# Optimization experiments

Hardware: AMD Instinct MI355X
Metric: run time of the kernel (lower is better)

Reference implementation:

```python
import jax, jax.numpy as jnp
import numpy as np

WS = 7
NUM_HEADS = 4


def setup_inputs() -> dict:
    key = jax.random.key(0)
    ks = jax.random.split(key, 5)
    C = 128
    return {
        "x": jax.random.normal(ks[0], (8, 222, 222, C), dtype=jnp.float32),
        "qkv_w": jax.random.normal(ks[1], (C, 3 * C), dtype=jnp.float32) * 0.02,
        "qkv_b": jax.random.normal(ks[2], (3 * C,), dtype=jnp.float32) * 0.02,
        "proj_w": jax.random.normal(ks[3], (C, C), dtype=jnp.float32) * 0.02,
        "proj_b": jax.random.normal(ks[4], (C,), dtype=jnp.float32) * 0.02,
    }


def reference(x, qkv_w, qkv_b, proj_w, proj_b):
    B, H, W, C = x.shape
    ws, nh = WS, NUM_HEADS
    hd = C // nh
    scale = hd ** (-0.5)
    pad_h = (ws - H % ws) % ws
    pad_w = (ws - W % ws) % ws
    xp = jnp.pad(x, ((0, 0), (0, pad_h), (0, pad_w), (0, 0)))
    Hp, Wp = H + pad_h, W + pad_w
    # window partition: [B,Hp,Wp,C] -> [nW, ws*ws, C]
    xw = xp.reshape(B, Hp // ws, ws, Wp // ws, ws, C)
    xw = xw.transpose(0, 1, 3, 2, 4, 5).reshape(-1, ws * ws, C)
    # qkv projection
    qkv = xw @ qkv_w + qkv_b  # [nW, 49, 3C]
    qkv = qkv.reshape(-1, ws * ws, 3, nh, hd).transpose(2, 0, 3, 1, 4)
    q, k, v = qkv[0], qkv[1], qkv[2]  # each [nW, nh, 49, hd]
    attn = jax.nn.softmax(jnp.einsum('whqd,whkd->whqk', q, k) * scale, axis=-1)
    out = jnp.einsum('whqk,whkd->whqd', attn, v)  # [nW, nh, 49, hd]
    out = out.transpose(0, 2, 1, 3).reshape(-1, ws * ws, C)
    out = out @ proj_w + proj_b
    # window reverse: [nW, ws*ws, C] -> [B, Hp, Wp, C]
    out = out.reshape(B, Hp // ws, Wp // ws, ws, ws, C)
    out = out.transpose(0, 1, 3, 2, 4, 5).reshape(B, Hp, Wp, C)
    return out[:, :H, :W, :]
```

## Files before the change

### kernel.cpp

```cpp
#include <hip/hip_runtime.h>
#include <stdint.h>

typedef __attribute__((ext_vector_type(8))) short bf16x8;
typedef __attribute__((ext_vector_type(4))) float f32x4;

#define IMG 222

__device__ __forceinline__ unsigned short f2bf(float f){
  unsigned int u = __float_as_uint(f);
  return (unsigned short)((u + 0x7fffu + ((u >> 16) & 1u)) >> 16);
}

__device__ __forceinline__ int sw128(int r, int c){ return r*128 + (c ^ ((r & 7) << 3)); }
__device__ __forceinline__ int sw64 (int r, int c){ return r*64  + (c ^ ((r & 7) << 3)); }

__global__ void prep_weights(const float* __restrict__ qkv_w,
                             const float* __restrict__ proj_w,
                             unsigned short* __restrict__ qwt,
                             unsigned short* __restrict__ pwt){
  int i = blockIdx.x * blockDim.x + threadIdx.x;
  if (i < 384*128){ int n = i >> 7, k = i & 127; qwt[i] = f2bf(qkv_w[k*384 + n]); }
  if (i < 128*128){ int n = i >> 7, k = i & 127; pwt[i] = f2bf(proj_w[k*128 + n]); }
}

__global__ __launch_bounds__(256, 3)
void win_attn(const float* __restrict__ x,
              const float* __restrict__ qkv_b,
              const float* __restrict__ proj_b,
              const unsigned short* __restrict__ qwt,
              const unsigned short* __restrict__ pwt,
              float* __restrict__ out)
{
  extern __shared__ unsigned short lds[];
  unsigned short* r0 = lds;
  unsigned short* r1 = lds + 8192;
  unsigned short* r2 = lds + 16384;

  const int tid = threadIdx.x;
  const int wid = tid >> 6;
  const int l   = tid & 63;
  const int l15 = l & 15;
  const int lhi = l >> 4;

  const int w  = (blockIdx.x & 7) * 1024 + (blockIdx.x >> 3);
  const int b  = w >> 10;
  const int wi = (w >> 5) & 31;
  const int wj = w & 31;

  {
    const int t  = tid >> 2;
    const int cb = (tid & 3) * 32;
    const int r  = t / 7, c = t - r*7;
    const int gh = wi*7 + r, gw = wj*7 + c;
    const bool valid = (t < 49) && (gh < IMG) && (gw < IMG);
    const float* src = x + (((size_t)((size_t)b*IMG + gh))*IMG + gw)*128 + cb;
    #pragma unroll
    for (int i = 0; i < 8; ++i){
      float4 v = valid ? *(const float4*)(src + i*4) : make_float4(0.f,0.f,0.f,0.f);
      *(ushort4*)(r0 + sw128(t, cb + i*4)) =
        make_ushort4(f2bf(v.x), f2bf(v.y), f2bf(v.z), f2bf(v.w));
    }
  }
  __syncthreads();

  bf16x8 a[4][4];
  #pragma unroll
  for (int mi = 0; mi < 4; ++mi)
    #pragma unroll
    for (int ks = 0; ks < 4; ++ks)
      a[mi][ks] = *(const bf16x8*)(r0 + sw128(mi*16 + l15, ks*32 + lhi*8));
  __syncthreads();

  const float scale = 0.17677669529663687f;

  #pragma unroll
  for (int nj = 0; nj < 6; ++nj){
    const int ni = wid + nj*4;
    bf16x8 bfr[4];
    #pragma unroll
    for (int ks = 0; ks < 4; ++ks)
      bfr[ks] = *(const bf16x8*)(qwt + (ni*16 + l15)*128 + ks*32 + lhi*8);
    if (nj < 4){
      const float4 bias4 = *(const float4*)(qkv_b + ni*16 + lhi*4);
      #pragma unroll
      for (int mi = 0; mi < 4; ++mi){
        f32x4 acc = {0.f,0.f,0.f,0.f};
        #pragma unroll
        for (int ks = 0; ks < 4; ++ks)
          acc = __builtin_amdgcn_mfma_f32_16x16x32_bf16(bfr[ks], a[mi][ks], acc, 0, 0, 0);
        if (nj < 2){
          *(ushort4*)(r0 + sw128(mi*16 + l15, ni*16 + lhi*4)) =
            make_ushort4(f2bf((acc[0]+bias4.x)*scale), f2bf((acc[1]+bias4.y)*scale),
                         f2bf((acc[2]+bias4.z)*scale), f2bf((acc[3]+bias4.w)*scale));
        } else {
          *(ushort4*)(r1 + sw128(mi*16 + l15, (ni-8)*16 + lhi*4)) =
            make_ushort4(f2bf(acc[0]+bias4.x), f2bf(acc[1]+bias4.y),
                         f2bf(acc[2]+bias4.z), f2bf(acc[3]+bias4.w));
        }
      }
    } else {
      const float bias = qkv_b[ni*16 + l15];
      #pragma unroll
      for (int mi = 0; mi < 4; ++mi){
        f32x4 acc = {0.f,0.f,0.f,0.f};
        #pragma unroll
        for (int ks = 0; ks < 4; ++ks)
          acc = __builtin_amdgcn_mfma_f32_16x16x32_bf16(a[mi][ks], bfr[ks], acc, 0, 0, 0);
        *(ushort4*)(r2 + sw64((ni-16)*16 + l15, mi*16 + lhi*4)) =
          make_ushort4(f2bf(acc[0]+bias), f2bf(acc[1]+bias),
                       f2bf(acc[2]+bias), f2bf(acc[3]+bias));
      }
    }
  }
  __syncthreads();

  const int h = wid;
  unsigned short* ph = lds + h*4096;
  bf16x8 aq[4], bk[4];
  #pragma unroll
  for (int i = 0; i < 4; ++i){
    aq[i] = *(const bf16x8*)(r0 + sw128(i*16 + l15, h*32 + lhi*8));
    bk[i] = *(const bf16x8*)(r1 + sw128(i*16 + l15, h*32 + lhi*8));
  }
  __syncthreads();

  float invs[4];
  #pragma unroll
  for (int mi = 0; mi < 4; ++mi){
    f32x4 st[4];
    #pragma unroll
    for (int ni = 0; ni < 4; ++ni){
      f32x4 z = {0.f,0.f,0.f,0.f};
      st[ni] = __builtin_amdgcn_mfma_f32_16x16x32_bf16(bk[ni], aq[mi], z, 0, 0, 0);
    }
    st[3][1] = -1e30f; st[3][2] = -1e30f; st[3][3] = -1e30f;
    if (lhi != 0) st[3][0] = -1e30f;
    float m = st[0][0];
    #pragma unroll
    for (int ni = 0; ni < 4; ++ni)
      #pragma unroll
      for (int r = 0; r < 4; ++r)
        m = fmaxf(m, st[ni][r]);
    m = fmaxf(m, __shfl_xor(m, 16));
    m = fmaxf(m, __shfl_xor(m, 32));
    float e[4][4], s = 0.f;
    #pragma unroll
    for (int ni = 0; ni < 4; ++ni)
      #pragma unroll
      for (int r = 0; r < 4; ++r){
        e[ni][r] = __expf(st[ni][r] - m);
        s += e[ni][r];
      }
    s += __shfl_xor(s, 16);
    s += __shfl_xor(s, 32);
    invs[mi] = __builtin_amdgcn_rcpf(s);
    #pragma unroll
    for (int ni = 0; ni < 4; ++ni)
      *(ushort4*)(ph + sw64(mi*16 + l15, ni*16 + lhi*4)) =
        make_ushort4(f2bf(e[ni][0]), f2bf(e[ni][1]), f2bf(e[ni][2]), f2bf(e[ni][3]));
  }

  bf16x8 pa[4][2], bv[2][2];
  #pragma unroll
  for (int mi = 0; mi < 4; ++mi)
    #pragma unroll
    for (int ks = 0; ks < 2; ++ks)
      pa[mi][ks] = *(const bf16x8*)(ph + sw64(mi*16 + l15, ks*32 + lhi*8));
  #pragma unroll
  for (int nc = 0; nc < 2; ++nc)
    #pragma unroll
    for (int ks = 0; ks < 2; ++ks)
      bv[nc][ks] = *(const bf16x8*)(r2 + sw64(h*32 + nc*16 + l15, ks*32 + lhi*8));
  __syncthreads();

  #pragma unroll
  for (int mi = 0; mi < 4; ++mi){
    const float is = invs[mi];
    #pragma unroll
    for (int nc = 0; nc < 2; ++nc){
      f32x4 acc = {0.f,0.f,0.f,0.f};
      acc = __builtin_amdgcn_mfma_f32_16x16x32_bf16(bv[nc][0], pa[mi][0], acc, 0, 0, 0);
      acc = __builtin_amdgcn_mfma_f32_16x16x32_bf16(bv[nc][1], pa[mi][1], acc, 0, 0, 0);
      *(ushort4*)(r2 + sw128(mi*16 + l15, h*32 + nc*16 + lhi*4)) =
        make_ushort4(f2bf(acc[0]*is), f2bf(acc[1]*is), f2bf(acc[2]*is), f2bf(acc[3]*is));
    }
  }
  __syncthreads();

  bf16x8 ao[4][4];
  #pragma unroll
  for (int mi = 0; mi < 4; ++mi)
    #pragma unroll
    for (int ks = 0; ks < 4; ++ks)
      ao[mi][ks] = *(const bf16x8*)(r2 + sw128(mi*16 + l15, ks*32 + lhi*8));

  #pragma unroll
  for (int nj = 0; nj < 2; ++nj){
    const int ni = wid + nj*4;
    bf16x8 pbw[4];
    #pragma unroll
    for (int ks = 0; ks < 4; ++ks)
      pbw[ks] = *(const bf16x8*)(pwt + (ni*16 + l15)*128 + ks*32 + lhi*8);
    const float4 bias4 = *(const float4*)(proj_b + ni*16 + lhi*4);
    #pragma unroll
    for (int mi = 0; mi < 4; ++mi){
      f32x4 acc = {0.f,0.f,0.f,0.f};
      #pragma unroll
      for (int ks = 0; ks < 4; ++ks)
        acc = __builtin_amdgcn_mfma_f32_16x16x32_bf16(pbw[ks], ao[mi][ks], acc, 0, 0, 0);
      const int t = mi*16 + l15;
      if (t < 49){
        const int rr = t / 7, cc = t - rr*7;
        const int gh = wi*7 + rr, gw = wj*7 + cc;
        if (gh < IMG && gw < IMG){
          float4 o = make_float4(acc[0]+bias4.x, acc[1]+bias4.y,
                                 acc[2]+bias4.z, acc[3]+bias4.w);
          *(float4*)(out + (((size_t)((size_t)b*IMG + gh))*IMG + gw)*128 + ni*16 + lhi*4) = o;
        }
      }
    }
  }
}

extern "C" void kernel_launch(void* const* d_in, const int* in_sizes, int n_in,
                              void* d_out, int out_size, void* d_ws, size_t ws_size,
                              hipStream_t stream) {
  const float* x      = (const float*)d_in[0];
  const float* qkv_w  = (const float*)d_in[1];
  const float* qkv_b  = (const float*)d_in[2];
  const float* proj_w = (const float*)d_in[3];
  const float* proj_b = (const float*)d_in[4];
  float* out = (float*)d_out;

  unsigned short* qwt = (unsigned short*)d_ws;
  unsigned short* pwt = qwt + 384*128;

  hipLaunchKernelGGL(prep_weights, dim3(192), dim3(256), 0, stream,
                     qkv_w, proj_w, qwt, pwt);
  hipLaunchKernelGGL(win_attn, dim3(8192), dim3(256), 49152, stream,
                     x, qkv_b, proj_b, qwt, pwt, out);
}
```

Before: 215.3 us.

## Keep half of V in registers via shuffles, shrink LDS, use packed bf16 converts

```diff
diff --git a/kernel.cpp b/kernel.cpp
--- a/kernel.cpp
+++ b/kernel.cpp
@@ -3,12 +3,19 @@
 
 typedef __attribute__((ext_vector_type(8))) short bf16x8;
 typedef __attribute__((ext_vector_type(4))) float f32x4;
+typedef __attribute__((ext_vector_type(4))) unsigned int u32x4;
 
 #define IMG 222
 
 __device__ __forceinline__ unsigned short f2bf(float f){
   unsigned int u = __float_as_uint(f);
   return (unsigned short)((u + 0x7fffu + ((u >> 16) & 1u)) >> 16);
+}
+
+__device__ __forceinline__ unsigned int pk2bf(float lo, float hi){
+  unsigned int r;
+  asm("v_cvt_pk_bf16_f32 %0, %1, %2" : "=v"(r) : "v"(lo), "v"(hi));
+  return r;
 }
 
 __device__ __forceinline__ int sw128(int r, int c){ return r*128 + (c ^ ((r & 7) << 3)); }
@@ -23,7 +30,7 @@
   if (i < 128*128){ int n = i >> 7, k = i & 127; pwt[i] = f2bf(proj_w[k*128 + n]); }
 }
 
-__global__ __launch_bounds__(256, 3)
+__global__ __launch_bounds__(256, 4)
 void win_attn(const float* __restrict__ x,
               const float* __restrict__ qkv_b,
               const float* __restrict__ proj_b,
@@ -57,8 +64,8 @@
     #pragma unroll
     for (int i = 0; i < 8; ++i){
       float4 v = valid ? *(const float4*)(src + i*4) : make_float4(0.f,0.f,0.f,0.f);
-      *(ushort4*)(r0 + sw128(t, cb + i*4)) =
-        make_ushort4(f2bf(v.x), f2bf(v.y), f2bf(v.z), f2bf(v.w));
+      uint2 pk; pk.x = pk2bf(v.x, v.y); pk.y = pk2bf(v.z, v.w);
+      *(uint2*)(r0 + sw128(t, cb + i*4)) = pk;
     }
   }
   __syncthreads();
@@ -74,42 +81,68 @@
   const float scale = 0.17677669529663687f;
 
   #pragma unroll
-  for (int nj = 0; nj < 6; ++nj){
-    const int ni = wid + nj*4;
+  for (int s = 0; s < 4; ++s){
+    const int nt = wid + s*4;
     bf16x8 bfr[4];
     #pragma unroll
     for (int ks = 0; ks < 4; ++ks)
-      bfr[ks] = *(const bf16x8*)(qwt + (ni*16 + l15)*128 + ks*32 + lhi*8);
-    if (nj < 4){
-      const float4 bias4 = *(const float4*)(qkv_b + ni*16 + lhi*4);
-      #pragma unroll
-      for (int mi = 0; mi < 4; ++mi){
-        f32x4 acc = {0.f,0.f,0.f,0.f};
-        #pragma unroll
-        for (int ks = 0; ks < 4; ++ks)
-          acc = __builtin_amdgcn_mfma_f32_16x16x32_bf16(bfr[ks], a[mi][ks], acc, 0, 0, 0);
-        if (nj < 2){
-          *(ushort4*)(r0 + sw128(mi*16 + l15, ni*16 + lhi*4)) =
-            make_ushort4(f2bf((acc[0]+bias4.x)*scale), f2bf((acc[1]+bias4.y)*scale),
-                         f2bf((acc[2]+bias4.z)*scale), f2bf((acc[3]+bias4.w)*scale));
-        } else {
-          *(ushort4*)(r1 + sw128(mi*16 + l15, (ni-8)*16 + lhi*4)) =
-            make_ushort4(f2bf(acc[0]+bias4.x), f2bf(acc[1]+bias4.y),
-                         f2bf(acc[2]+bias4.z), f2bf(acc[3]+bias4.w));
-        }
-      }
-    } else {
-      const float bias = qkv_b[ni*16 + l15];
-      #pragma unroll
-      for (int mi = 0; mi < 4; ++mi){
-        f32x4 acc = {0.f,0.f,0.f,0.f};
-        #pragma unroll
-        for (int ks = 0; ks < 4; ++ks)
-          acc = __builtin_amdgcn_mfma_f32_16x16x32_bf16(a[mi][ks], bfr[ks], acc, 0, 0, 0);
-        *(ushort4*)(r2 + sw64((ni-16)*16 + l15, mi*16 + lhi*4)) =
-          make_ushort4(f2bf(acc[0]+bias), f2bf(acc[1]+bias),
-                       f2bf(acc[2]+bias), f2bf(acc[3]+bias));
-      }
+      bfr[ks] = *(const bf16x8*)(qwt + (nt*16 + l15)*128 + ks*32 + lhi*8);
+    const float4 bias4 = *(const float4*)(qkv_b + nt*16 + lhi*4);
+    #pragma unroll
+    for (int mi = 0; mi < 4; ++mi){
+      f32x4 acc = {0.f,0.f,0.f,0.f};
+      #pragma unroll
+      for (int ks = 0; ks < 4; ++ks)
+        acc = __builtin_amdgcn_mfma_f32_16x16x32_bf16(bfr[ks], a[mi][ks], acc, 0, 0, 0);
+      uint2 pk;
+      if (s < 2){
+        pk.x = pk2bf((acc[0]+bias4.x)*scale, (acc[1]+bias4.y)*scale);
+        pk.y = pk2bf((acc[2]+bias4.z)*scale, (acc[3]+bias4.w)*scale);
+        *(uint2*)(r0 + sw128(mi*16 + l15, nt*16 + lhi*4)) = pk;
+      } else {
+        pk.x = pk2bf(acc[0]+bias4.x, acc[1]+bias4.y);
+        pk.y = pk2bf(acc[2]+bias4.z, acc[3]+bias4.w);
+        *(uint2*)(r1 + sw128(mi*16 + l15, (nt-8)*16 + lhi*4)) = pk;
+      }
+    }
+  }
+
+  unsigned int pkv[4][2];
+  {
+    const int nt0 = 16 + 2*wid;
+    bf16x8 bfr[4];
+    #pragma unroll
+    for (int ks = 0; ks < 4; ++ks)
+      bfr[ks] = *(const bf16x8*)(qwt + (nt0*16 + l15)*128 + ks*32 + lhi*8);
+    const float bias = qkv_b[nt0*16 + l15];
+    #pragma unroll
+    for (int mi = 0; mi < 4; ++mi){
+      f32x4 acc = {0.f,0.f,0.f,0.f};
+      #pragma unroll
+      for (int ks = 0; ks < 4; ++ks)
+        acc = __builtin_amdgcn_mfma_f32_16x16x32_bf16(a[mi][ks], bfr[ks], acc, 0, 0, 0);
+      pkv[mi][0] = pk2bf(acc[0]+bias, acc[1]+bias);
+      pkv[mi][1] = pk2bf(acc[2]+bias, acc[3]+bias);
+    }
+  }
+  {
+    const int nt1 = 17 + 2*wid;
+    bf16x8 bfr[4];
+    #pragma unroll
+    for (int ks = 0; ks < 4; ++ks)
+      bfr[ks] = *(const bf16x8*)(qwt + (nt1*16 + l15)*128 + ks*32 + lhi*8);
+    const float bias = qkv_b[nt1*16 + l15];
+    unsigned short* vh = r2 + wid*1024;
+    #pragma unroll
+    for (int mi = 0; mi < 4; ++mi){
+      f32x4 acc = {0.f,0.f,0.f,0.f};
+      #pragma unroll
+      for (int ks = 0; ks < 4; ++ks)
+        acc = __builtin_amdgcn_mfma_f32_16x16x32_bf16(a[mi][ks], bfr[ks], acc, 0, 0, 0);
+      uint2 pk;
+      pk.x = pk2bf(acc[0]+bias, acc[1]+bias);
+      pk.y = pk2bf(acc[2]+bias, acc[3]+bias);
+      *(uint2*)(vh + sw64(l15, mi*16 + lhi*4)) = pk;
     }
   }
   __syncthreads();
@@ -155,22 +188,43 @@
     s += __shfl_xor(s, 32);
     invs[mi] = __builtin_amdgcn_rcpf(s);
     #pragma unroll
-    for (int ni = 0; ni < 4; ++ni)
-      *(ushort4*)(ph + sw64(mi*16 + l15, ni*16 + lhi*4)) =
-        make_ushort4(f2bf(e[ni][0]), f2bf(e[ni][1]), f2bf(e[ni][2]), f2bf(e[ni][3]));
-  }
-
-  bf16x8 pa[4][2], bv[2][2];
+    for (int ni = 0; ni < 4; ++ni){
+      uint2 pk;
+      pk.x = pk2bf(e[ni][0], e[ni][1]);
+      pk.y = pk2bf(e[ni][2], e[ni][3]);
+      *(uint2*)(ph + sw64(mi*16 + l15, ni*16 + lhi*4)) = pk;
+    }
+  }
+
+  bf16x8 pa[4][2];
   #pragma unroll
   for (int mi = 0; mi < 4; ++mi)
     #pragma unroll
     for (int ks = 0; ks < 2; ++ks)
       pa[mi][ks] = *(const bf16x8*)(ph + sw64(mi*16 + l15, ks*32 + lhi*8));
-  #pragma unroll
-  for (int nc = 0; nc < 2; ++nc)
+  bf16x8 bv1[2];
+  {
+    unsigned short* vh = r2 + wid*1024;
     #pragma unroll
     for (int ks = 0; ks < 2; ++ks)
-      bv[nc][ks] = *(const bf16x8*)(r2 + sw64(h*32 + nc*16 + l15, ks*32 + lhi*8));
+      bv1[ks] = *(const bf16x8*)(vh + sw64(l15, ks*32 + lhi*8));
+  }
+  bf16x8 bv0[2];
+  {
+    const int srcA = ((l & 16) << 1) + l15;
+    #pragma unroll
+    for (int ks = 0; ks < 2; ++ks){
+      u32x4 wv;
+      #pragma unroll
+      for (int jj = 0; jj < 4; ++jj){
+        const int src = srcA + ((jj >> 1) << 4);
+        unsigned int va = (unsigned int)__shfl((int)pkv[2*ks][jj & 1], src);
+        unsigned int vb = (unsigned int)__shfl((int)pkv[2*ks+1][jj & 1], src);
+        wv[jj] = (lhi & 2) ? vb : va;
+      }
+      bv0[ks] = __builtin_bit_cast(bf16x8, wv);
+    }
+  }
   __syncthreads();
 
   #pragma unroll
@@ -179,10 +233,12 @@
     #pragma unroll
     for (int nc = 0; nc < 2; ++nc){
       f32x4 acc = {0.f,0.f,0.f,0.f};
-      acc = __builtin_amdgcn_mfma_f32_16x16x32_bf16(bv[nc][0], pa[mi][0], acc, 0, 0, 0);
-      acc = __builtin_amdgcn_mfma_f32_16x16x32_bf16(bv[nc][1], pa[mi][1], acc, 0, 0, 0);
-      *(ushort4*)(r2 + sw128(mi*16 + l15, h*32 + nc*16 + lhi*4)) =
-        make_ushort4(f2bf(acc[0]*is), f2bf(acc[1]*is), f2bf(acc[2]*is), f2bf(acc[3]*is));
+      acc = __builtin_amdgcn_mfma_f32_16x16x32_bf16(nc ? bv1[0] : bv0[0], pa[mi][0], acc, 0, 0, 0);
+      acc = __builtin_amdgcn_mfma_f32_16x16x32_bf16(nc ? bv1[1] : bv0[1], pa[mi][1], acc, 0, 0, 0);
+      uint2 pk;
+      pk.x = pk2bf(acc[0]*is, acc[1]*is);
+      pk.y = pk2bf(acc[2]*is, acc[3]*is);
+      *(uint2*)(r0 + sw128(mi*16 + l15, h*32 + nc*16 + lhi*4)) = pk;
     }
   }
   __syncthreads();
@@ -192,7 +248,7 @@
   for (int mi = 0; mi < 4; ++mi)
     #pragma unroll
     for (int ks = 0; ks < 4; ++ks)
-      ao[mi][ks] = *(const bf16x8*)(r2 + sw128(mi*16 + l15, ks*32 + lhi*8));
+      ao[mi][ks] = *(const bf16x8*)(r0 + sw128(mi*16 + l15, ks*32 + lhi*8));
 
   #pragma unroll
   for (int nj = 0; nj < 2; ++nj){
@@ -237,6 +293,6 @@
 
   hipLaunchKernelGGL(prep_weights, dim3(192), dim3(256), 0, stream,
                      qkv_w, proj_w, qwt, pwt);
-  hipLaunchKernelGGL(win_attn, dim3(8192), dim3(256), 49152, stream,
+  hipLaunchKernelGGL(win_attn, dim3(8192), dim3(256), 40960, stream,
                      x, qkv_b, proj_b, qwt, pwt, out);
 }
```

New measurement: 207.3 us. 1.04x faster.
